# Optimization experiments

Hardware: AMD Instinct MI355X
Metric: run time of the kernel (lower is better)

Reference implementation:

```python
import jax, jax.numpy as jnp
import numpy as np

SIZE = 11
SIGMA = 1.5
ALPHA = 0.7
K1 = 0.01
K2 = 0.03
DATA_RANGE = 1.0
DN = ('NCDHW', 'OIDHW', 'NCDHW')


def _gauss1d():
    ax = jnp.arange(SIZE, dtype=jnp.float32) - SIZE // 2
    k = jnp.exp(-(ax ** 2) / (2.0 * SIGMA * SIGMA))
    return k / k.sum()


def _blur3d(x, k1):
    # Separable depthwise 3D gaussian blur with zero ('constant') padding.
    # Mathematically identical to the dense 11x11x11 outer-product conv3d
    # in the torch source (zero padding commutes with separable passes).
    ch = x.shape[1]
    pad = SIZE // 2
    for kshape in ((SIZE, 1, 1), (1, SIZE, 1), (1, 1, SIZE)):
        w = jnp.broadcast_to(k1.reshape(1, 1, *kshape), (ch, 1) + kshape)
        pads = [(pad, pad) if s == SIZE else (0, 0) for s in kshape]
        x = jax.lax.conv_general_dilated(
            x, w, window_strides=(1, 1, 1), padding=pads,
            dimension_numbers=DN, feature_group_count=ch)
    return x


def setup_inputs() -> dict:
    key = jax.random.key(0)
    k1, k2 = jax.random.split(key)
    shape = (2, 1, 160, 160, 160)
    pred = jax.random.uniform(k1, shape, dtype=jnp.float32)
    target = jax.random.uniform(k2, shape, dtype=jnp.float32)
    return {"pred": pred, "target": target}


def reference(pred, target):
    k1d = _gauss1d()
    pred32 = pred.astype(jnp.float32)
    target32 = target.astype(jnp.float32)

    # L1
    l1 = jnp.mean(jnp.abs(pred32 - target32))

    # SSIM3D
    mu1 = _blur3d(pred32, k1d)
    mu2 = _blur3d(target32, k1d)
    mu1_sq = mu1 * mu1
    mu2_sq = mu2 * mu2
    mu1_mu2 = mu1 * mu2
    sigma1_sq = _blur3d(pred32 * pred32, k1d) - mu1_sq
    sigma2_sq = _blur3d(target32 * target32, k1d) - mu2_sq
    sigma12 = _blur3d(pred32 * target32, k1d) - mu1_mu2

    C1 = (K1 * DATA_RANGE) ** 2
    C2 = (K2 * DATA_RANGE) ** 2
    ssim_map = ((2.0 * mu1_mu2 + C1) * (2.0 * sigma12 + C2)) / (
        (mu1_sq + mu2_sq + C1) * (sigma1_sq + sigma2_sq + C2) + 1e-12)
    ssim = jnp.mean(ssim_map)

    return ALPHA * l1 + (1.0 - ALPHA) * (1.0 - ssim)
```

## Files before the change

kernel.cpp:

```cpp
#include <hip/hip_runtime.h>

#define DHW 160
#define PLANE (160*160)
#define VOL (160*160*160)
#define PAD 5
#define KS 11
#define TXW 16
#define TYH 32
#define LZ 32
#define SRX 26
#define SRY 42
#define SRP 48
#define XBP 24
#define NSLOT 5
#define STAGE_NP (SRY*SRX)
#define NITER ((LZ + 2*PAD) / 2)
#define NBLOCKS 500
#define CNT_POISON 0xAAAAAAAAu

__device__ __forceinline__ void gauss_w(float w[KS]) {
    float s = 0.f;
#pragma unroll
    for (int i = 0; i < KS; ++i) {
        float d = (float)(i - PAD);
        w[i] = expf(-(d * d) / (2.f * 1.5f * 1.5f));
        s += w[i];
    }
    float inv = 1.f / s;
#pragma unroll
    for (int i = 0; i < KS; ++i) w[i] *= inv;
}

__device__ __forceinline__ float block_reduce(float v, float* sm) {
#pragma unroll
    for (int off = 32; off > 0; off >>= 1)
        v += __shfl_down(v, off);
    int lane = threadIdx.x & 63;
    int wid  = threadIdx.x >> 6;
    if (lane == 0) sm[wid] = v;
    __syncthreads();
    float r = 0.f;
    if (threadIdx.x == 0) r = sm[0] + sm[1] + sm[2] + sm[3];
    return r;
}

__global__ __launch_bounds__(256, 2) void k_fused(
    const float* __restrict__ pred, const float* __restrict__ targ,
    double* __restrict__ accum, unsigned* __restrict__ cnt,
    float* __restrict__ out)
{
    __shared__ __align__(16) float sIn[2][2][SRY][SRP];
    __shared__ __align__(16) float sXB[2][5][SRY][XBP];
    __shared__ float sRed[4];

    float gw[KS]; gauss_w(gw);

    const int tile = blockIdx.x;
    const int xt = tile % 10, yt = tile / 10;
    const int z0 = blockIdx.y * LZ;
    const int b  = blockIdx.z;
    const float* __restrict__ P = pred + (size_t)b * VOL;
    const float* __restrict__ T = targ + (size_t)b * VOL;
    const ptrdiff_t dTP = T - P;

    const int tid = threadIdx.x;
    const int tx  = tid & 15;
    const int ty2 = tid >> 4;
    const int y0  = 2 * ty2;

    const float* sptrP[NSLOT];
    int  soff[NSLOT];
    bool sact[NSLOT];
    bool sl1[NSLOT];
#pragma unroll
    for (int i = 0; i < NSLOT; ++i) {
        int idx = tid + 256 * i;
        bool act = idx < STAGE_NP;
        int idc = act ? idx : 0;
        int r   = idc / SRX;
        int c   = idc - r * SRX;
        int gy = yt * TYH + r - PAD;
        int gx = xt * TXW + c - PAD;
        bool inp = (gy >= 0 && gy < DHW && gx >= 0 && gx < DHW);
        sact[i] = act && inp;
        sl1[i]  = act && (r >= PAD && r < PAD + TYH) && (c >= PAD && c < PAD + TXW);
        soff[i] = r * SRP + c;
        sptrP[i] = P + (inp ? (gy * DHW + gx) : 0);
    }

    auto stage_fetch = [&](int zz, float vp[NSLOT], float vt[NSLOT]) {
        bool zok = (zz >= 0 && zz < DHW);
        size_t zo = (size_t)(zok ? zz : 0) * PLANE;
#pragma unroll
        for (int i = 0; i < NSLOT; ++i) {
            bool ok = zok && sact[i];
            vp[i] = ok ? sptrP[i][zo] : 0.f;
            vt[i] = ok ? sptrP[i][zo + dTP] : 0.f;
        }
    };
    auto stage_write = [&](int slice, const float vp[NSLOT], const float vt[NSLOT]) {
        float* basep = &sIn[slice][0][0][0];
        float* baset = &sIn[slice][1][0][0];
#pragma unroll
        for (int i = 0; i < NSLOT; ++i)
            if (tid + 256 * i < STAGE_NP) {
                basep[soff[i]] = vp[i];
                baset[soff[i]] = vt[i];
            }
    };

    auto xblur_unit = [&](int s, int r4, int cg) {
        const float4* rp = (const float4*)&sIn[s][0][r4][0];
        const float4* rt = (const float4*)&sIn[s][1][r4][0];
        float4 a0 = rp[cg], a1 = rp[cg + 1], a2 = rp[cg + 2], a3 = rp[cg + 3];
        float4 b0 = rt[cg], b1 = rt[cg + 1], b2 = rt[cg + 2], b3 = rt[cg + 3];
        float pv[16] = {a0.x,a0.y,a0.z,a0.w, a1.x,a1.y,a1.z,a1.w,
                        a2.x,a2.y,a2.z,a2.w, a3.x,a3.y,a3.z,a3.w};
        float tv[16] = {b0.x,b0.y,b0.z,b0.w, b1.x,b1.y,b1.z,b1.w,
                        b2.x,b2.y,b2.z,b2.w, b3.x,b3.y,b3.z,b3.w};
        float pp[14], tt2[14], pt2[14];
#pragma unroll
        for (int i = 0; i < 14; ++i) {
            pp[i]  = pv[i] * pv[i];
            tt2[i] = tv[i] * tv[i];
            pt2[i] = pv[i] * tv[i];
        }
        float o[5][4];
#pragma unroll
        for (int oo = 0; oo < 4; ++oo) {
            float s0 = 0, s1 = 0, s2 = 0, s3 = 0, s4 = 0;
#pragma unroll
            for (int j = 0; j < KS; ++j) {
                float w = gw[j];
                s0 += w * pv[oo + j];
                s1 += w * tv[oo + j];
                s2 += w * pp[oo + j];
                s3 += w * tt2[oo + j];
                s4 += w * pt2[oo + j];
            }
            o[0][oo] = s0; o[1][oo] = s1; o[2][oo] = s2;
            o[3][oo] = s3; o[4][oo] = s4;
        }
#pragma unroll
        for (int f = 0; f < 5; ++f) {
            float4 w4 = make_float4(o[f][0], o[f][1], o[f][2], o[f][3]);
            ((float4*)&sXB[s][f][r4][0])[cg] = w4;
        }
    };

    float pend[2][5][KS];
#pragma unroll
    for (int o = 0; o < 2; ++o)
#pragma unroll
        for (int f = 0; f < 5; ++f)
#pragma unroll
            for (int j = 0; j < KS; ++j) pend[o][f][j] = 0.f;

    float l1s = 0.f, sss = 0.f;

    const float C1 = 0.01f * 0.01f;
    const float C2 = 0.03f * 0.03f;

    auto yblur_push = [&](int s, bool doEmit) {
        float v[2][5];
#pragma unroll
        for (int f = 0; f < 5; ++f) {
            float tap[KS + 1];
#pragma unroll
            for (int j = 0; j < KS + 1; ++j)
                tap[j] = sXB[s][f][y0 + j][tx];
            float a0 = 0.f, a1 = 0.f;
#pragma unroll
            for (int j = 0; j < KS; ++j) {
                float w = gw[j];
                a0 += w * tap[j];
                a1 += w * tap[j + 1];
            }
            v[0][f] = a0;
            v[1][f] = a1;
        }
#pragma unroll
        for (int o = 0; o < 2; ++o) {
#pragma unroll
            for (int i = 0; i < KS - 1; ++i) {
                float w = gw[10 - i];
#pragma unroll
                for (int f = 0; f < 5; ++f)
                    pend[o][f][i] = pend[o][f][i + 1] + w * v[o][f];
            }
#pragma unroll
            for (int f = 0; f < 5; ++f)
                pend[o][f][10] = gw[0] * v[o][f];
        }
        if (doEmit) {
#pragma unroll
            for (int o = 0; o < 2; ++o) {
                float m1 = pend[o][0][0], m2 = pend[o][1][0];
                float e11 = pend[o][2][0], e22 = pend[o][3][0], e12 = pend[o][4][0];
                float mu11 = m1 * m1, mu22 = m2 * m2, mu12 = m1 * m2;
                float s1 = e11 - mu11, s2 = e22 - mu22, s12 = e12 - mu12;
                float num = (2.f * mu12 + C1) * (2.f * s12 + C2);
                float den = (mu11 + mu22 + C1) * (s1 + s2 + C2) + 1e-12f;
                sss += num / den;
            }
        }
    };

    {
        float vp[NSLOT], vt[NSLOT];
        stage_fetch(z0 - PAD, vp, vt);
        stage_write(0, vp, vt);
        stage_fetch(z0 - PAD + 1, vp, vt);
        stage_write(1, vp, vt);
    }
    __syncthreads();

    for (int m = 0; m < NITER; ++m) {
        const int jA = 2 * m + 2, jB = 2 * m + 3;
        float pA[NSLOT], tA[NSLOT], pB[NSLOT], tB[NSLOT];
        const bool doStage = (m < NITER - 1);

        if (doStage) {
            stage_fetch(z0 - PAD + jA, pA, tA);
            stage_fetch(z0 - PAD + jB, pB, tB);
            if ((unsigned)(jA - PAD) < (unsigned)LZ) {
#pragma unroll
                for (int i = 0; i < NSLOT; ++i)
                    if (sl1[i]) l1s += fabsf(pA[i] - tA[i]);
            }
            if ((unsigned)(jB - PAD) < (unsigned)LZ) {
#pragma unroll
                for (int i = 0; i < NSLOT; ++i)
                    if (sl1[i]) l1s += fabsf(pB[i] - tB[i]);
            }
        }

        {
            int u = tid;
            int s = u / 168, rem = u - s * 168;
            xblur_unit(s, rem >> 2, rem & 3);
            if (tid < 336 - 256) {
                int u2 = tid + 256;
                int rem2 = u2 - 168;
                xblur_unit(1, rem2 >> 2, rem2 & 3);
            }
        }

        __syncthreads();

        if (doStage) {
            stage_write(0, pA, tA);
            stage_write(1, pB, tB);
        }

        const bool em = (m >= 5);
        yblur_push(0, em);
        yblur_push(1, em);

        __syncthreads();
    }

    float r1 = block_reduce(l1s, sRed);
    __syncthreads();
    float r2 = block_reduce(sss, sRed);
    if (tid == 0) {
        atomicAdd(&accum[0], (double)r1);
        atomicAdd(&accum[1], (double)r2);
        __threadfence();
        unsigned prev = atomicAdd(cnt, 1u);
        if (prev == CNT_POISON + (unsigned)NBLOCKS - 1u) {
            const double n = 8192000.0;
            double l1   = atomicAdd(&accum[0], 0.0) / n;
            double ssim = atomicAdd(&accum[1], 0.0) / n;
            out[0] = (float)(0.7 * l1 + 0.3 * (1.0 - ssim));
        }
    }
}

extern "C" void kernel_launch(void* const* d_in, const int* in_sizes, int n_in,
                              void* d_out, int out_size, void* d_ws, size_t ws_size,
                              hipStream_t stream) {
    const float* pred = (const float*)d_in[0];
    const float* targ = (const float*)d_in[1];
    float* out = (float*)d_out;
    double* accum = (double*)d_ws;
    unsigned* cnt = (unsigned*)((char*)d_ws + 64);

    dim3 grid(50, DHW / LZ, 2);
    k_fused<<<grid, 256, 0, stream>>>(pred, targ, accum, cnt, out);
}
```

Before: 198.4 us.

## Interleave pred/target in shared memory and use packed float2 FMA math

Shared-memory staging now stores pred and target interleaved as float2 pairs, and the x-blur outputs are split into paired arrays (mu1/mu2, e11/e22) plus a scalar e12 array. The x-blur, y-blur and z-pending accumulators use 2-wide vector types so the compiler can emit packed FMA instructions, which is meant to cut FP32 instruction count. In exchange, the padding of the shared rows changes, which can alter LDS bank-conflict behaviour, and the vector register layout may raise register pressure.

```diff
diff --git a/kernel.cpp b/kernel.cpp
--- a/kernel.cpp
+++ b/kernel.cpp
@@ -1,4 +1,6 @@
 #include <hip/hip_runtime.h>
+
+typedef float v2f __attribute__((ext_vector_type(2)));
 
 #define DHW 160
 #define PLANE (160*160)
@@ -10,8 +12,8 @@
 #define LZ 32
 #define SRX 26
 #define SRY 42
-#define SRP 48
-#define XBP 24
+#define XA2 18
+#define XC  24
 #define NSLOT 5
 #define STAGE_NP (SRY*SRX)
 #define NITER ((LZ + 2*PAD) / 2)
@@ -49,8 +51,10 @@
     double* __restrict__ accum, unsigned* __restrict__ cnt,
     float* __restrict__ out)
 {
-    __shared__ __align__(16) float sIn[2][2][SRY][SRP];
-    __shared__ __align__(16) float sXB[2][5][SRY][XBP];
+    __shared__ __align__(16) v2f   sIn[2][SRY][SRX];
+    __shared__ __align__(16) v2f   sXBa[2][SRY][XA2];
+    __shared__ __align__(16) v2f   sXBb[2][SRY][XA2];
+    __shared__ __align__(16) float sXBc[2][SRY][XC];
     __shared__ float sRed[4];
 
     float gw[KS]; gauss_w(gw);
@@ -69,7 +73,6 @@
     const int y0  = 2 * ty2;
 
     const float* sptrP[NSLOT];
-    int  soff[NSLOT];
     bool sact[NSLOT];
     bool sl1[NSLOT];
 #pragma unroll
@@ -84,7 +87,6 @@
         bool inp = (gy >= 0 && gy < DHW && gx >= 0 && gx < DHW);
         sact[i] = act && inp;
         sl1[i]  = act && (r >= PAD && r < PAD + TYH) && (c >= PAD && c < PAD + TXW);
-        soff[i] = r * SRP + c;
         sptrP[i] = P + (inp ? (gy * DHW + gx) : 0);
     }
 
@@ -99,106 +101,112 @@
         }
     };
     auto stage_write = [&](int slice, const float vp[NSLOT], const float vt[NSLOT]) {
-        float* basep = &sIn[slice][0][0][0];
-        float* baset = &sIn[slice][1][0][0];
-#pragma unroll
-        for (int i = 0; i < NSLOT; ++i)
-            if (tid + 256 * i < STAGE_NP) {
-                basep[soff[i]] = vp[i];
-                baset[soff[i]] = vt[i];
-            }
+        v2f* base = &sIn[slice][0][0];
+#pragma unroll
+        for (int i = 0; i < NSLOT; ++i) {
+            int idx = tid + 256 * i;
+            if (idx < STAGE_NP) {
+                v2f w; w.x = vp[i]; w.y = vt[i];
+                base[idx] = w;
+            }
+        }
     };
 
     auto xblur_unit = [&](int s, int r4, int cg) {
-        const float4* rp = (const float4*)&sIn[s][0][r4][0];
-        const float4* rt = (const float4*)&sIn[s][1][r4][0];
-        float4 a0 = rp[cg], a1 = rp[cg + 1], a2 = rp[cg + 2], a3 = rp[cg + 3];
-        float4 b0 = rt[cg], b1 = rt[cg + 1], b2 = rt[cg + 2], b3 = rt[cg + 3];
-        float pv[16] = {a0.x,a0.y,a0.z,a0.w, a1.x,a1.y,a1.z,a1.w,
-                        a2.x,a2.y,a2.z,a2.w, a3.x,a3.y,a3.z,a3.w};
-        float tv[16] = {b0.x,b0.y,b0.z,b0.w, b1.x,b1.y,b1.z,b1.w,
-                        b2.x,b2.y,b2.z,b2.w, b3.x,b3.y,b3.z,b3.w};
-        float pp[14], tt2[14], pt2[14];
+        const float4* row = (const float4*)&sIn[s][r4][0];
+        v2f pt[14];
+#pragma unroll
+        for (int m = 0; m < 7; ++m) {
+            float4 q = row[2 * cg + m];
+            v2f lo; lo.x = q.x; lo.y = q.y;
+            v2f hi; hi.x = q.z; hi.y = q.w;
+            pt[2 * m]     = lo;
+            pt[2 * m + 1] = hi;
+        }
+        v2f mm[14]; float pc[14];
 #pragma unroll
         for (int i = 0; i < 14; ++i) {
-            pp[i]  = pv[i] * pv[i];
-            tt2[i] = tv[i] * tv[i];
-            pt2[i] = pv[i] * tv[i];
-        }
-        float o[5][4];
-#pragma unroll
-        for (int oo = 0; oo < 4; ++oo) {
-            float s0 = 0, s1 = 0, s2 = 0, s3 = 0, s4 = 0;
-#pragma unroll
-            for (int j = 0; j < KS; ++j) {
-                float w = gw[j];
-                s0 += w * pv[oo + j];
-                s1 += w * tv[oo + j];
-                s2 += w * pp[oo + j];
-                s3 += w * tt2[oo + j];
-                s4 += w * pt2[oo + j];
-            }
-            o[0][oo] = s0; o[1][oo] = s1; o[2][oo] = s2;
-            o[3][oo] = s3; o[4][oo] = s4;
-        }
-#pragma unroll
-        for (int f = 0; f < 5; ++f) {
-            float4 w4 = make_float4(o[f][0], o[f][1], o[f][2], o[f][3]);
-            ((float4*)&sXB[s][f][r4][0])[cg] = w4;
-        }
-    };
-
-    float pend[2][5][KS];
+            mm[i] = pt[i] * pt[i];
+            pc[i] = pt[i].x * pt[i].y;
+        }
+        v2f a01[4], a23[4]; float a4[4];
+#pragma unroll
+        for (int oo = 0; oo < 4; ++oo) { a01[oo] = 0.f; a23[oo] = 0.f; a4[oo] = 0.f; }
+#pragma unroll
+        for (int j = 0; j < KS; ++j) {
+            float w = gw[j];
+#pragma unroll
+            for (int oo = 0; oo < 4; ++oo) {
+                a01[oo] += pt[oo + j] * w;
+                a23[oo] += mm[oo + j] * w;
+                a4[oo]  += pc[oo + j] * w;
+            }
+        }
+        float4* wa = (float4*)&sXBa[s][r4][0];
+        float4 qa0, qa1;
+        qa0.x = a01[0].x; qa0.y = a01[0].y; qa0.z = a01[1].x; qa0.w = a01[1].y;
+        qa1.x = a01[2].x; qa1.y = a01[2].y; qa1.z = a01[3].x; qa1.w = a01[3].y;
+        wa[2 * cg] = qa0; wa[2 * cg + 1] = qa1;
+        float4* wb = (float4*)&sXBb[s][r4][0];
+        float4 qb0, qb1;
+        qb0.x = a23[0].x; qb0.y = a23[0].y; qb0.z = a23[1].x; qb0.w = a23[1].y;
+        qb1.x = a23[2].x; qb1.y = a23[2].y; qb1.z = a23[3].x; qb1.w = a23[3].y;
+        wb[2 * cg] = qb0; wb[2 * cg + 1] = qb1;
+        float4* wc = (float4*)&sXBc[s][r4][0];
+        float4 qc; qc.x = a4[0]; qc.y = a4[1]; qc.z = a4[2]; qc.w = a4[3];
+        wc[cg] = qc;
+    };
+
+    v2f pend01[2][KS], pend23[2][KS];
+    float pend4[2][KS];
 #pragma unroll
     for (int o = 0; o < 2; ++o)
 #pragma unroll
-        for (int f = 0; f < 5; ++f)
-#pragma unroll
-            for (int j = 0; j < KS; ++j) pend[o][f][j] = 0.f;
+        for (int j = 0; j < KS; ++j) {
+            pend01[o][j] = 0.f; pend23[o][j] = 0.f; pend4[o][j] = 0.f;
+        }
 
     float l1s = 0.f, sss = 0.f;
-
     const float C1 = 0.01f * 0.01f;
     const float C2 = 0.03f * 0.03f;
 
     auto yblur_push = [&](int s, bool doEmit) {
-        float v[2][5];
-#pragma unroll
-        for (int f = 0; f < 5; ++f) {
-            float tap[KS + 1];
-#pragma unroll
-            for (int j = 0; j < KS + 1; ++j)
-                tap[j] = sXB[s][f][y0 + j][tx];
-            float a0 = 0.f, a1 = 0.f;
-#pragma unroll
-            for (int j = 0; j < KS; ++j) {
-                float w = gw[j];
-                a0 += w * tap[j];
-                a1 += w * tap[j + 1];
-            }
-            v[0][f] = a0;
-            v[1][f] = a1;
+        v2f t01[KS + 1], t23[KS + 1]; float t4[KS + 1];
+#pragma unroll
+        for (int j = 0; j < KS + 1; ++j) {
+            t01[j] = sXBa[s][y0 + j][tx];
+            t23[j] = sXBb[s][y0 + j][tx];
+            t4[j]  = sXBc[s][y0 + j][tx];
+        }
+        v2f a01[2], a23[2]; float a4[2];
+        a01[0] = 0.f; a01[1] = 0.f; a23[0] = 0.f; a23[1] = 0.f; a4[0] = 0.f; a4[1] = 0.f;
+#pragma unroll
+        for (int j = 0; j < KS; ++j) {
+            float w = gw[j];
+            a01[0] += t01[j] * w;  a01[1] += t01[j + 1] * w;
+            a23[0] += t23[j] * w;  a23[1] += t23[j + 1] * w;
+            a4[0]  += t4[j]  * w;  a4[1]  += t4[j + 1]  * w;
         }
 #pragma unroll
         for (int o = 0; o < 2; ++o) {
 #pragma unroll
             for (int i = 0; i < KS - 1; ++i) {
                 float w = gw[10 - i];
-#pragma unroll
-                for (int f = 0; f < 5; ++f)
-                    pend[o][f][i] = pend[o][f][i + 1] + w * v[o][f];
-            }
-#pragma unroll
-            for (int f = 0; f < 5; ++f)
-                pend[o][f][10] = gw[0] * v[o][f];
+                pend01[o][i] = pend01[o][i + 1] + a01[o] * w;
+                pend23[o][i] = pend23[o][i + 1] + a23[o] * w;
+                pend4[o][i]  = pend4[o][i + 1]  + a4[o]  * w;
+            }
+            pend01[o][10] = a01[o] * gw[0];
+            pend23[o][10] = a23[o] * gw[0];
+            pend4[o][10]  = a4[o]  * gw[0];
         }
         if (doEmit) {
 #pragma unroll
             for (int o = 0; o < 2; ++o) {
-                float m1 = pend[o][0][0], m2 = pend[o][1][0];
-                float e11 = pend[o][2][0], e22 = pend[o][3][0], e12 = pend[o][4][0];
-                float mu11 = m1 * m1, mu22 = m2 * m2, mu12 = m1 * m2;
-                float s1 = e11 - mu11, s2 = e22 - mu22, s12 = e12 - mu12;
+                v2f m = pend01[o][0], e = pend23[o][0];
+                float e12 = pend4[o][0];
+                float mu11 = m.x * m.x, mu22 = m.y * m.y, mu12 = m.x * m.y;
+                float s1 = e.x - mu11, s2 = e.y - mu22, s12 = e12 - mu12;
                 float num = (2.f * mu12 + C1) * (2.f * s12 + C2);
                 float den = (mu11 + mu22 + C1) * (s1 + s2 + C2) + 1e-12f;
                 sss += num / den;
@@ -240,8 +248,7 @@
             int s = u / 168, rem = u - s * 168;
             xblur_unit(s, rem >> 2, rem & 3);
             if (tid < 336 - 256) {
-                int u2 = tid + 256;
-                int rem2 = u2 - 168;
+                int rem2 = tid + 256 - 168;
                 xblur_unit(1, rem2 >> 2, rem2 & 3);
             }
         }
```

Measured after the change: 181.8 us. -8.3%, faster.
